# Kernel tuning notes

Hardware: AMD Instinct MI355X
Metric: run time of the kernel (lower is better)

## Reference

```python
import jax, jax.numpy as jnp
import numpy as np

B, S, H = 2, 2048, 4096
NH, NKV, HD = 32, 8, 128
THETA = 1000000.0
NEG = jnp.finfo(jnp.float32).min


def setup_inputs() -> dict:
    key = jax.random.key(0)
    ks = jax.random.split(key, 9)
    s = 0.02
    return {
        "hidden_states": jax.random.normal(ks[0], (B, S, H), jnp.float32),
        "position_ids": jnp.tile(jnp.arange(S, dtype=jnp.int32)[None, :], (B, 1)),
        "Wq": jax.random.normal(ks[1], (NH * HD, H), jnp.float32) * s,
        "bq": jax.random.normal(ks[2], (NH * HD,), jnp.float32) * s,
        "Wk": jax.random.normal(ks[3], (NKV * HD, H), jnp.float32) * s,
        "bk": jax.random.normal(ks[4], (NKV * HD,), jnp.float32) * s,
        "Wv": jax.random.normal(ks[5], (NKV * HD, H), jnp.float32) * s,
        "bv": jax.random.normal(ks[6], (NKV * HD,), jnp.float32) * s,
        "Wo": jax.random.normal(ks[7], (H, H), jnp.float32) * s,
        "bo": jax.random.normal(ks[8], (H,), jnp.float32) * s,
    }


def _rotate_half_interleaved(x):
    # y[..., ::2] = -x[..., 1::2]; y[..., 1::2] = x[..., ::2]
    x2 = x.reshape(*x.shape[:-1], -1, 2)
    y = jnp.stack([-x2[..., 1], x2[..., 0]], axis=-1)
    return y.reshape(x.shape)


def reference(hidden_states, position_ids, Wq, bq, Wk, bk, Wv, bv, Wo, bo):
    bsz, q_len, _ = hidden_states.shape
    q = (hidden_states @ Wq.T + bq).reshape(bsz, q_len, NH, HD).transpose(0, 2, 1, 3)
    k = (hidden_states @ Wk.T + bk).reshape(bsz, q_len, NKV, HD).transpose(0, 2, 1, 3)
    v = (hidden_states @ Wv.T + bv).reshape(bsz, q_len, NKV, HD).transpose(0, 2, 1, 3)

    # rotary embedding (interleaved / repeat_interleave variant)
    inv_freq = 1.0 / (THETA ** (jnp.arange(0, HD, 2, dtype=jnp.float32) / HD))
    freqs = position_ids.astype(jnp.float32)[:, :, None] * inv_freq[None, None, :]  # [B,S,HD/2]
    emb = jnp.repeat(freqs, 2, axis=-1)  # [B,S,HD]
    cos = jnp.cos(emb)[:, None, :, :]  # [B,1,S,HD]
    sin = jnp.sin(emb)[:, None, :, :]
    q = q * cos + _rotate_half_interleaved(q) * sin
    k = k * cos + _rotate_half_interleaved(k) * sin

    # GQA: repeat KV heads (repeat_interleave on head axis)
    n_rep = NH // NKV
    k = jnp.repeat(k, n_rep, axis=1)
    v = jnp.repeat(v, n_rep, axis=1)

    scores = jnp.einsum("bhqd,bhkd->bhqk", q, k) / np.sqrt(HD).astype(np.float32)
    causal = jnp.tril(jnp.ones((q_len, q_len), dtype=bool))
    scores = jnp.where(causal[None, None, :, :], scores, NEG)
    attn = jax.nn.softmax(scores.astype(jnp.float32), axis=-1).astype(q.dtype)
    out = jnp.einsum("bhqk,bhkd->bhqd", attn, v)
    out = out.transpose(0, 2, 1, 3).reshape(bsz, q_len, H)
    return out @ Wo.T + bo
```

## Files before the change

### kernel.cpp

```cpp
#include <hip/hip_runtime.h>
#include <stdint.h>

typedef __bf16 bf16x8 __attribute__((ext_vector_type(8)));
typedef float f32x4 __attribute__((ext_vector_type(4)));
typedef float f32x16 __attribute__((ext_vector_type(16)));

#define S_LEN 2048
#define NKVH 8
#define HDIM 128
#define MROWS 4096
#define LDQKV 6144
#define SCALE 0.08838834764831845f
#define C_LOG2 0.1275405707067851f
#define THR_RAW 62.7f

__device__ __forceinline__ unsigned short f2bf(float f) {
  unsigned u = __float_as_uint(f);
  u += 0x7FFFu + ((u >> 16) & 1u);
  return (unsigned short)(u >> 16);
}
__device__ __forceinline__ float bf2f(unsigned short h) {
  return __uint_as_float(((unsigned)h) << 16);
}

__device__ __forceinline__ void gload16(const unsigned short* g, unsigned short* l) {
  __builtin_amdgcn_global_load_lds(
      (__attribute__((address_space(1))) void*)(g),
      (__attribute__((address_space(3))) void*)(l), 16, 0, 0);
}

__global__ void cast_f32_bf16(const float4* __restrict__ in, ushort4* __restrict__ out, int n4) {
  int i = blockIdx.x * 256 + threadIdx.x;
  const int stride = gridDim.x * 256;
  for (; i < n4; i += stride) {
    float4 v = in[i];
    ushort4 o;
    o.x = f2bf(v.x); o.y = f2bf(v.y); o.z = f2bf(v.z); o.w = f2bf(v.w);
    out[i] = o;
  }
}

template <int OUTF>
__global__ __launch_bounds__(512, 2)
void gemm256(const unsigned short* __restrict__ A,
             const unsigned short* __restrict__ Bw,
             const float* __restrict__ bias,
             void* __restrict__ C,
             int ldc, int K) {
  __shared__ unsigned short lds[2][4][8192];

  const int t = threadIdx.x;
  const int lane = t & 63;
  const int w = t >> 6;
  const int wr = w >> 2, wc = w & 3;
  const int row16 = lane & 15, kgrp = lane >> 4;
  const int m0 = blockIdx.y * 256, n0 = blockIdx.x * 256;

  const int riu = t >> 3;
  const int col = (((t & 7) ^ (riu & 7)) << 3);
  const int rB0 = (riu & 31) + ((riu >> 5) << 6);
  const unsigned short* pA = A + (size_t)(m0 + riu) * K + col;
  const unsigned short* pB = Bw + (size_t)(n0 + rB0) * K + col;

#define STG(nb_, u_, src_)                                                  \
  {                                                                         \
    gload16((src_), &lds[nb_][u_][t * 8]);                                  \
    gload16((src_) + (size_t)128 * K, &lds[nb_][u_][4096 + t * 8]);         \
  }

  const int sw = row16 & 7;
  const int abase = (wr * 64 + row16) * 64;
  const int bbase = (wc * 32 + row16) * 64;

  f32x4 acc[8][4];
#pragma unroll
  for (int i = 0; i < 8; i++)
#pragma unroll
    for (int j = 0; j < 4; j++) acc[i][j] = (f32x4){0.f, 0.f, 0.f, 0.f};

  bf16x8 afr[4][2], bfr[2][2][2];
  const int NT = K >> 6;

  STG(0, 0, pA);
  STG(0, 1, pB);
  STG(0, 2, pB + (size_t)32 * K);
  STG(0, 3, pA + (size_t)64 * K);

  for (int T = 0; T < NT; ++T) {
    const int cb = T & 1, nb = cb ^ 1;
    const unsigned short* Lc = &lds[cb][0][0];
    const size_t kk = (size_t)(T + 1) << 6;
    const bool st = (T + 1 < NT);

    asm volatile("s_waitcnt vmcnt(4)\n\ts_barrier" ::: "memory");
    if (st) STG(nb, 0, pA + kk);
#pragma unroll
    for (int mi = 0; mi < 4; mi++)
#pragma unroll
      for (int ks = 0; ks < 2; ks++)
        afr[mi][ks] = *(const bf16x8*)(Lc + abase + mi * 1024 + ((((ks << 2) + kgrp) ^ sw) << 3));
#pragma unroll
    for (int nj = 0; nj < 2; nj++)
#pragma unroll
      for (int ks = 0; ks < 2; ks++)
        bfr[0][nj][ks] = *(const bf16x8*)(Lc + 8192 + bbase + nj * 1024 + ((((ks << 2) + kgrp) ^ sw) << 3));
    __builtin_amdgcn_s_setprio(1);
#pragma unroll
    for (int mi = 0; mi < 4; mi++)
#pragma unroll
      for (int nj = 0; nj < 2; nj++)
#pragma unroll
        for (int ks = 0; ks < 2; ks++)
          acc[mi][nj] = __builtin_amdgcn_mfma_f32_16x16x32_bf16(afr[mi][ks], bfr[0][nj][ks], acc[mi][nj], 0, 0, 0);
    __builtin_amdgcn_s_setprio(0);

    if (st) {
      asm volatile("s_waitcnt vmcnt(4)\n\ts_barrier" ::: "memory");
      STG(nb, 1, pB + kk);
    } else {
      asm volatile("s_waitcnt vmcnt(2)\n\ts_barrier" ::: "memory");
    }
#pragma unroll
    for (int nj = 0; nj < 2; nj++)
#pragma unroll
      for (int ks = 0; ks < 2; ks++)
        bfr[1][nj][ks] = *(const bf16x8*)(Lc + 16384 + bbase + nj * 1024 + ((((ks << 2) + kgrp) ^ sw) << 3));
    __builtin_amdgcn_s_setprio(1);
#pragma unroll
    for (int mi = 0; mi < 4; mi++)
#pragma unroll
      for (int nj = 0; nj < 2; nj++)
#pragma unroll
        for (int ks = 0; ks < 2; ks++)
          acc[mi][2 + nj] = __builtin_amdgcn_mfma_f32_16x16x32_bf16(afr[mi][ks], bfr[1][nj][ks], acc[mi][2 + nj], 0, 0, 0);
    __builtin_amdgcn_s_setprio(0);

    if (st) {
      asm volatile("s_waitcnt vmcnt(4)\n\ts_barrier" ::: "memory");
      STG(nb, 2, pB + (size_t)32 * K + kk);
    } else {
      asm volatile("s_waitcnt vmcnt(0)\n\ts_barrier" ::: "memory");
    }
#pragma unroll
    for (int mi = 0; mi < 4; mi++)
#pragma unroll
      for (int ks = 0; ks < 2; ks++)
        afr[mi][ks] = *(const bf16x8*)(Lc + 24576 + abase + mi * 1024 + ((((ks << 2) + kgrp) ^ sw) << 3));
    __builtin_amdgcn_s_setprio(1);
#pragma unroll
    for (int mi = 0; mi < 4; mi++)
#pragma unroll
      for (int nj = 0; nj < 2; nj++)
#pragma unroll
        for (int ks = 0; ks < 2; ks++)
          acc[4 + mi][2 + nj] = __builtin_amdgcn_mfma_f32_16x16x32_bf16(afr[mi][ks], bfr[1][nj][ks], acc[4 + mi][2 + nj], 0, 0, 0);
    __builtin_amdgcn_s_setprio(0);

    if (st) {
      asm volatile("s_waitcnt vmcnt(4)\n\ts_barrier" ::: "memory");
      STG(nb, 3, pA + (size_t)64 * K + kk);
    } else {
      asm volatile("s_barrier" ::: "memory");
    }
    __builtin_amdgcn_s_setprio(1);
#pragma unroll
    for (int mi = 0; mi < 4; mi++)
#pragma unroll
      for (int nj = 0; nj < 2; nj++)
#pragma unroll
        for (int ks = 0; ks < 2; ks++)
          acc[4 + mi][nj] = __builtin_amdgcn_mfma_f32_16x16x32_bf16(afr[mi][ks], bfr[0][nj][ks], acc[4 + mi][nj], 0, 0, 0);
    __builtin_amdgcn_s_setprio(0);
  }
#undef STG

#pragma unroll
  for (int MI = 0; MI < 8; MI++) {
#pragma unroll
    for (int NJ = 0; NJ < 4; NJ++) {
      const int gr = m0 + wr * 128 + MI * 16 + kgrp * 4;
      const int gc = n0 + wc * 64 + NJ * 16 + row16;
      const float bv = bias[gc];
#pragma unroll
      for (int jj = 0; jj < 4; jj++) {
        float v = acc[MI][NJ][jj] + bv;
        if (OUTF) ((float*)C)[(size_t)(gr + jj) * ldc + gc] = v;
        else ((unsigned short*)C)[(size_t)(gr + jj) * ldc + gc] = f2bf(v);
      }
    }
  }
}

template <int OUTF>
__global__ __launch_bounds__(512, 2)
void gemm128(const unsigned short* __restrict__ A,
             const unsigned short* __restrict__ Bw,
             const float* __restrict__ bias,
             void* __restrict__ C,
             int ldc, int K) {
  __shared__ unsigned short lds[3 * 24576];

  const int t = threadIdx.x;
  const int lane = t & 63;
  const int w = t >> 6;
  const int wr = w >> 2, wc = w & 3;
  const int row16 = lane & 15, kgrp = lane >> 4;
  const int m0 = blockIdx.y * 128, n0 = blockIdx.x * 256;

  const int riu = t >> 3;
  const int col = (((t & 7) ^ (riu & 7)) << 3);
  const unsigned short* pA = A + (size_t)(m0 + riu) * K + col;
  const unsigned short* pB = Bw + (size_t)(n0 + riu) * K + col;

#define STG6(bo_, kk_)                                                      \
  {                                                                         \
    gload16(pA + (kk_), &lds[(bo_) + t * 8]);                               \
    gload16(pA + (size_t)64 * K + (kk_), &lds[(bo_) + 4096 + t * 8]);       \
    gload16(pB + (kk_), &lds[(bo_) + 8192 + t * 8]);                        \
    gload16(pB + (size_t)64 * K + (kk_), &lds[(bo_) + 12288 + t * 8]);      \
    gload16(pB + (size_t)128 * K + (kk_), &lds[(bo_) + 16384 + t * 8]);     \
    gload16(pB + (size_t)192 * K + (kk_), &lds[(bo_) + 20480 + t * 8]);     \
  }

  const int sw = row16 & 7;
  const int abase = (wr * 64 + row16) * 64;
  const int bbase = 8192 + (wc * 64 + row16) * 64;

  f32x4 acc[4][4];
#pragma unroll
  for (int i = 0; i < 4; i++)
#pragma unroll
    for (int j = 0; j < 4; j++) acc[i][j] = (f32x4){0.f, 0.f, 0.f, 0.f};

  bf16x8 afr[4][2], bfr[4][2];
  const int NT = K >> 6;

  STG6(0, 0);
  STG6(24576, 64);

  int rbc = 0;
  int rbs = 2;
  for (int T = 0; T < NT; ++T) {
    if (T < NT - 1) { asm volatile("s_waitcnt vmcnt(6)\n\ts_barrier" ::: "memory"); }
    else            { asm volatile("s_waitcnt vmcnt(0)\n\ts_barrier" ::: "memory"); }
    if (T + 2 < NT) STG6(rbs * 24576, (size_t)(T + 2) << 6);
    const unsigned short* Lc = &lds[rbc * 24576];

#pragma unroll
    for (int mi = 0; mi < 4; mi++)
#pragma unroll
      for (int ks = 0; ks < 2; ks++)
        afr[mi][ks] = *(const bf16x8*)(Lc + abase + mi * 1024 + ((((ks << 2) + kgrp) ^ sw) << 3));
#pragma unroll
    for (int nj = 0; nj < 4; nj++)
#pragma unroll
      for (int ks = 0; ks < 2; ks++)
        bfr[nj][ks] = *(const bf16x8*)(Lc + bbase + nj * 1024 + ((((ks << 2) + kgrp) ^ sw) << 3));

    __builtin_amdgcn_s_setprio(1);
#pragma unroll
    for (int mi = 0; mi < 4; mi++)
#pragma unroll
      for (int nj = 0; nj < 4; nj++)
#pragma unroll
        for (int ks = 0; ks < 2; ks++)
          acc[mi][nj] = __builtin_amdgcn_mfma_f32_16x16x32_bf16(afr[mi][ks], bfr[nj][ks], acc[mi][nj], 0, 0, 0);
    __builtin_amdgcn_s_setprio(0);

    rbc++; if (rbc == 3) rbc = 0;
    rbs++; if (rbs == 3) rbs = 0;
  }
#undef STG6

#pragma unroll
  for (int MI = 0; MI < 4; MI++) {
#pragma unroll
    for (int NJ = 0; NJ < 4; NJ++) {
      const int gr = m0 + wr * 64 + MI * 16 + kgrp * 4;
      const int gc = n0 + wc * 64 + NJ * 16 + row16;
      const float bv = bias[gc];
#pragma unroll
      for (int jj = 0; jj < 4; jj++) {
        float v = acc[MI][NJ][jj] + bv;
        if (OUTF) ((float*)C)[(size_t)(gr + jj) * ldc + gc] = v;
        else ((unsigned short*)C)[(size_t)(gr + jj) * ldc + gc] = f2bf(v);
      }
    }
  }
}

__global__ void rope_kernel(unsigned short* __restrict__ X,
                            const int* __restrict__ pos_ids,
                            int ncols, int ld) {
  const int perrow = ncols >> 3;
  int idx = blockIdx.x * 256 + threadIdx.x;
  const int row = idx / perrow;
  const int c0 = (idx - row * perrow) << 3;
  const float pos = (float)pos_ids[row];
  unsigned short* p = X + (size_t)row * ld + c0;
  uint4 v = *(uint4*)p;
  unsigned short* e = (unsigned short*)&v;
  const int p0 = (c0 & 127) >> 1;
#pragma unroll
  for (int q = 0; q < 4; ++q) {
    const float inv = exp2f(-(float)(p0 + q) * (19.931568569324174f / 64.f));
    const float fr = pos * inv;
    float sn, cs;
    __sincosf(fr, &sn, &cs);
    const float xe = bf2f(e[2 * q]);
    const float xo = bf2f(e[2 * q + 1]);
    e[2 * q]     = f2bf(xe * cs - xo * sn);
    e[2 * q + 1] = f2bf(xo * cs + xe * sn);
  }
  *(uint4*)p = v;
}

__global__ void transpose_v(const unsigned short* __restrict__ V, int ldv,
                            unsigned short* __restrict__ Vt) {
  __shared__ unsigned short tile[32][40];
  const int t = threadIdx.x;
  const int n0 = blockIdx.x * 32;
  const int m0 = blockIdx.y * 32;
  const int r = t >> 3;
  const int c = (t & 7) << 2;
  const unsigned short* src = V + (size_t)(m0 + r) * ldv + n0 + c;
  ushort4 d = *(const ushort4*)src;
  tile[r][c] = d.x; tile[r][c + 1] = d.y; tile[r][c + 2] = d.z; tile[r][c + 3] = d.w;
  __syncthreads();
  const int b = m0 >> 11;
  unsigned short* dst = Vt + (size_t)(b * 1024 + n0 + r) * 2048 + (m0 & 2047) + c;
  ushort4 o;
  o.x = tile[c][r]; o.y = tile[c + 1][r]; o.z = tile[c + 2][r]; o.w = tile[c + 3][r];
  *(ushort4*)dst = o;
}

__global__ __launch_bounds__(256, 2)
void attn_kernel3(const unsigned short* __restrict__ QKV,
                  const unsigned short* __restrict__ Vt,
                  unsigned short* __restrict__ O) {
  __shared__ unsigned short sK[2 * 64 * 128];
  __shared__ unsigned short sV[2 * 128 * 64];

  const int t = threadIdx.x;
  const int lane = t & 63;
  const int w = t >> 6;
  const int l31 = lane & 31;
  const int hi = lane >> 5;
  const int bid = blockIdx.x;
  const int g = bid >> 6, bh = bid & 63;
  const int qt = (g < 8) ? (15 - g) : (g - 8);
  const int b = bh >> 5, h = bh & 31;
  const int kh = h >> 2;
  const int q0 = qt << 7;
  const int qw = q0 + w * 32;
  const int qg = qw + l31;

  const int ntiles = (q0 + 128) >> 6;
  const int myTiles = (qw + 95) >> 6;

  const int krow0 = t >> 4;
  const int kslot = t & 15;
  const int vrow0 = t >> 3;
  const int vslot = t & 7;
  const unsigned short* Kp = QKV + (size_t)(b * S_LEN) * LDQKV + 4096 + kh * HDIM;
  const unsigned short* Vp = Vt + (size_t)(b * 1024 + kh * HDIM) * 2048;
  const int ksw = (kslot ^ (krow0 & 7)) << 3;
  const int vsw = (vslot ^ (vrow0 & 7)) << 3;
  const unsigned short* KpA = Kp + (size_t)krow0 * LDQKV + ksw;
  const unsigned short* VpA = Vp + (size_t)vrow0 * 2048 + vsw;

#define STAGE(bufi, kv0m)                                                      \
  {                                                                            \
    _Pragma("unroll")                                                          \
    for (int p = 0; p < 4; p++)                                                \
      gload16(KpA + (size_t)((kv0m) + 16 * p) * LDQKV,                         \
              &sK[(bufi) * 8192 + p * 2048 + t * 8]);                          \
    _Pragma("unroll")                                                          \
    for (int p = 0; p < 4; p++)                                                \
      gload16(VpA + (kv0m) + p * 65536, &sV[(bufi) * 8192 + p * 2048 + t * 8]); \
  }

  bf16x8 qf[8];
  {
    const unsigned short* qb = QKV + (size_t)(b * S_LEN + qw + l31) * LDQKV + h * HDIM + hi * 8;
#pragma unroll
    for (int kd = 0; kd < 8; kd++) qf[kd] = *(const bf16x8*)(qb + kd * 16);
  }

  f32x16 o[4];
#pragma unroll
  for (int nt = 0; nt < 4; nt++)
#pragma unroll
    for (int r = 0; r < 16; r++) o[nt][r] = 0.f;
  float m = -1e30f, lsum = 0.f;

  const int rw7 = (l31 & 7) << 4;
  const int kswz = (hi << 4) ^ rw7;
  const int kbase0 = l31 * 128;
  const int vbase = l31 * 64;

  STAGE(0, 0);
  int buf = 0;
  for (int it = 0; it < ntiles; ++it) {
    if (it + 1 < ntiles) {
      STAGE(buf ^ 1, (it + 1) << 6);
      asm volatile("s_waitcnt vmcnt(8)" ::: "memory");
    } else {
      asm volatile("s_waitcnt vmcnt(0)" ::: "memory");
    }
    __builtin_amdgcn_s_barrier();

    if (it < myTiles) {
      const unsigned short* sKc = sK + buf * 8192;
      const unsigned short* sVc = sV + buf * 8192;
      const int kv0 = it << 6;

      f32x16 st[2];
#pragma unroll
      for (int r = 0; r < 16; r++) { st[0][r] = 0.f; st[1][r] = 0.f; }
      __builtin_amdgcn_s_setprio(1);
#pragma unroll
      for (int kd = 0; kd < 8; kd++) {
        bf16x8 k0 = *(const bf16x8*)(sKc + kbase0 + (((kd << 5) ^ kswz) >> 1));
        bf16x8 k1 = *(const bf16x8*)(sKc + 4096 + kbase0 + (((kd << 5) ^ kswz) >> 1));
        st[0] = __builtin_amdgcn_mfma_f32_32x32x16_bf16(k0, qf[kd], st[0], 0, 0, 0);
        st[1] = __builtin_amdgcn_mfma_f32_32x32x16_bf16(k1, qf[kd], st[1], 0, 0, 0);
      }
      __builtin_amdgcn_s_setprio(0);

      if (it == myTiles - 1) {
#pragma unroll
        for (int s2 = 0; s2 < 2; s2++)
#pragma unroll
          for (int r = 0; r < 16; r++) {
            const int kvg = kv0 + s2 * 32 + (r & 3) + 8 * (r >> 2) + 4 * hi;
            if (kvg > qg) st[s2][r] = -1e30f;
          }
      }

      float mx[8];
#pragma unroll
      for (int r = 0; r < 8; r++)
        mx[r] = fmaxf(fmaxf(st[0][r], st[0][r + 8]), fmaxf(st[1][r], st[1][r + 8]));
#pragma unroll
      for (int d = 4; d >= 1; d >>= 1)
#pragma unroll
        for (int r = 0; r < d; r++) mx[r] = fmaxf(mx[r], mx[r + d]);
      float tmax = fmaxf(mx[0], __shfl_xor(mx[0], 32));

      if (!__all(tmax <= m + THR_RAW)) {
        const float mnew = fmaxf(m, tmax);
        const float corr = exp2f((m - mnew) * C_LOG2);
        lsum *= corr;
#pragma unroll
        for (int r = 0; r < 16; r++) {
          const int src = (r & 3) + 8 * (r >> 2) + 4 * hi;
          const float cr = __shfl(corr, src);
#pragma unroll
          for (int nt = 0; nt < 4; nt++) o[nt][r] *= cr;
        }
        m = mnew;
      }
      const float mC = m * C_LOG2;

#pragma unroll
      for (int s2 = 0; s2 < 2; s2++)
#pragma unroll
        for (int r = 0; r < 16; r++) st[s2][r] = exp2f(fmaf(st[s2][r], C_LOG2, -mC));
      float sm[8];
#pragma unroll
      for (int r = 0; r < 8; r++)
        sm[r] = (st[0][r] + st[0][r + 8]) + (st[1][r] + st[1][r + 8]);
#pragma unroll
      for (int d = 4; d >= 1; d >>= 1)
#pragma unroll
        for (int r = 0; r < d; r++) sm[r] += sm[r + d];
      float tsum = sm[0] + __shfl_xor(sm[0], 32);
      lsum += tsum;

      bf16x8 pa[4];
#pragma unroll
      for (int s2 = 0; s2 < 2; s2++) {
        unsigned pw[8];
#pragma unroll
        for (int i = 0; i < 8; i++)
          asm("v_cvt_pk_bf16_f32 %0, %1, %2" : "=v"(pw[i]) : "v"(st[s2][2 * i]), "v"(st[s2][2 * i + 1]));
        const unsigned x0 = (unsigned)__shfl_xor((int)pw[0], 32);
        const unsigned x1 = (unsigned)__shfl_xor((int)pw[1], 32);
        const unsigned x2 = (unsigned)__shfl_xor((int)pw[2], 32);
        const unsigned x3 = (unsigned)__shfl_xor((int)pw[3], 32);
        const unsigned x4 = (unsigned)__shfl_xor((int)pw[4], 32);
        const unsigned x5 = (unsigned)__shfl_xor((int)pw[5], 32);
        const unsigned x6 = (unsigned)__shfl_xor((int)pw[6], 32);
        const unsigned x7 = (unsigned)__shfl_xor((int)pw[7], 32);
        union { unsigned u[4]; bf16x8 v; } u0, u1;
        u0.u[0] = hi ? x2 : pw[0];
        u0.u[1] = hi ? x3 : pw[1];
        u0.u[2] = hi ? pw[2] : x0;
        u0.u[3] = hi ? pw[3] : x1;
        u1.u[0] = hi ? x6 : pw[4];
        u1.u[1] = hi ? x7 : pw[5];
        u1.u[2] = hi ? pw[6] : x4;
        u1.u[3] = hi ? pw[7] : x5;
        pa[2 * s2] = u0.v; pa[2 * s2 + 1] = u1.v;
      }

      __builtin_amdgcn_s_setprio(1);
#pragma unroll
      for (int nt = 0; nt < 4; nt++) {
        const unsigned short* vr = sVc + vbase + nt * 2048;
#pragma unroll
        for (int ks = 0; ks < 4; ks++) {
          bf16x8 vb = *(const bf16x8*)(vr + (((ks << 5) ^ kswz) >> 1));
          o[nt] = __builtin_amdgcn_mfma_f32_32x32x16_bf16(pa[ks], vb, o[nt], 0, 0, 0);
        }
      }
      __builtin_amdgcn_s_setprio(0);
    }

    __builtin_amdgcn_s_barrier();
    buf ^= 1;
  }

  const float linv = 1.0f / lsum;
#pragma unroll
  for (int r = 0; r < 16; r++) {
    const int qr = (r & 3) + 8 * (r >> 2) + 4 * hi;
    const float lr = __shfl(linv, qr);
    unsigned short* orow = O + (size_t)(b * S_LEN + qw + qr) * 4096 + h * HDIM + l31;
#pragma unroll
    for (int nt = 0; nt < 4; nt++) orow[nt * 32] = f2bf(o[nt][r] * lr);
  }
#undef STAGE
}

extern "C" void kernel_launch(void* const* d_in, const int* in_sizes, int n_in,
                              void* d_out, int out_size, void* d_ws, size_t ws_size,
                              hipStream_t stream) {
  const float* hs = (const float*)d_in[0];
  const int*  pos = (const int*)d_in[1];
  const float* Wq = (const float*)d_in[2];
  const float* bq = (const float*)d_in[3];
  const float* Wk = (const float*)d_in[4];
  const float* bk = (const float*)d_in[5];
  const float* Wv = (const float*)d_in[6];
  const float* bv = (const float*)d_in[7];
  const float* Wo = (const float*)d_in[8];
  const float* bo = (const float*)d_in[9];
  float* out = (float*)d_out;

  char* ws = (char*)d_ws;
  unsigned short* hbf  = (unsigned short*)(ws);
  unsigned short* Wbuf = (unsigned short*)(ws + 33554432);
  unsigned short* QKV  = (unsigned short*)(ws + 83886080);
  unsigned short* Vtb  = (unsigned short*)(ws + 134217728);
  float*          biasb= (float*)(ws + 142606336);

  cast_f32_bf16<<<2048, 256, 0, stream>>>((const float4*)hs, (ushort4*)hbf, 4194304);
  cast_f32_bf16<<<2048, 256, 0, stream>>>((const float4*)Wq, (ushort4*)Wbuf, 4194304);
  cast_f32_bf16<<<1024, 256, 0, stream>>>((const float4*)Wk, (ushort4*)(Wbuf + 16777216), 1048576);
  cast_f32_bf16<<<1024, 256, 0, stream>>>((const float4*)Wv, (ushort4*)(Wbuf + 20971520), 1048576);
  hipMemcpyAsync(biasb, bq, 4096 * 4, hipMemcpyDeviceToDevice, stream);
  hipMemcpyAsync(biasb + 4096, bk, 1024 * 4, hipMemcpyDeviceToDevice, stream);
  hipMemcpyAsync(biasb + 5120, bv, 1024 * 4, hipMemcpyDeviceToDevice, stream);

  gemm256<0><<<dim3(16, 16), 512, 0, stream>>>(hbf, Wbuf, biasb, QKV, LDQKV, 4096);
  gemm128<0><<<dim3(8, 32), 512, 0, stream>>>(hbf, Wbuf + 16777216, biasb + 4096, QKV + 4096, LDQKV, 4096);

  cast_f32_bf16<<<2048, 256, 0, stream>>>((const float4*)Wo, (ushort4*)Wbuf, 4194304);

  rope_kernel<<<8192, 256, 0, stream>>>(QKV, pos, 4096, LDQKV);
  rope_kernel<<<2048, 256, 0, stream>>>(QKV + 4096, pos, 1024, LDQKV);

  transpose_v<<<dim3(32, 128), 256, 0, stream>>>(QKV + 5120, LDQKV, Vtb);

  attn_kernel3<<<dim3(1024), 256, 0, stream>>>(QKV, Vtb, hbf);

  gemm256<1><<<dim3(16, 16), 512, 0, stream>>>(hbf, Wbuf, bo, out, 4096, 4096);
}
```

Measured before the change: 520.8 us.

## Restructure GEMM mainloop into 8-slot LDS ring with deeper prefetch

```diff
diff --git a/kernel.cpp b/kernel.cpp
--- a/kernel.cpp
+++ b/kernel.cpp
@@ -47,7 +47,7 @@
              const float* __restrict__ bias,
              void* __restrict__ C,
              int ldc, int K) {
-  __shared__ unsigned short lds[2][4][8192];
+  __shared__ unsigned short lds[8][8192];
 
   const int t = threadIdx.x;
   const int lane = t & 63;
@@ -62,11 +62,30 @@
   const unsigned short* pA = A + (size_t)(m0 + riu) * K + col;
   const unsigned short* pB = Bw + (size_t)(n0 + rB0) * K + col;
 
-#define STG(nb_, u_, src_)                                                  \
+#define STGU(SL, SRC)                                                       \
   {                                                                         \
-    gload16((src_), &lds[nb_][u_][t * 8]);                                  \
-    gload16((src_) + (size_t)128 * K, &lds[nb_][u_][4096 + t * 8]);         \
-  }
+    gload16((SRC), &lds[SL][t * 8]);                                        \
+    gload16((SRC) + (size_t)128 * K, &lds[SL][4096 + t * 8]);               \
+  }
+#define RDA(SL)                                                             \
+  _Pragma("unroll") for (int mi = 0; mi < 4; mi++)                          \
+  _Pragma("unroll") for (int ks = 0; ks < 2; ks++)                          \
+    afr[mi][ks] = *(const bf16x8*)(&lds[SL][0] + abase + mi * 1024 +        \
+                                   ((((ks << 2) + kgrp) ^ sw) << 3));
+#define RDB(SL, W)                                                          \
+  _Pragma("unroll") for (int nj = 0; nj < 2; nj++)                          \
+  _Pragma("unroll") for (int ks = 0; ks < 2; ks++)                          \
+    bfr[W][nj][ks] = *(const bf16x8*)(&lds[SL][0] + bbase + nj * 1024 +     \
+                                      ((((ks << 2) + kgrp) ^ sw) << 3));
+#define MM(MO, NO, W)                                                       \
+  __builtin_amdgcn_s_setprio(1);                                            \
+  _Pragma("unroll") for (int mi = 0; mi < 4; mi++)                          \
+  _Pragma("unroll") for (int nj = 0; nj < 2; nj++)                          \
+  _Pragma("unroll") for (int ks = 0; ks < 2; ks++)                          \
+    acc[(MO) + mi][(NO) + nj] = __builtin_amdgcn_mfma_f32_16x16x32_bf16(    \
+        afr[mi][ks], bfr[W][nj][ks], acc[(MO) + mi][(NO) + nj], 0, 0, 0);   \
+  __builtin_amdgcn_s_setprio(0);
+#define BAR __builtin_amdgcn_s_barrier()
 
   const int sw = row16 & 7;
   const int abase = (wr * 64 + row16) * 64;
@@ -80,99 +99,78 @@
 
   bf16x8 afr[4][2], bfr[2][2][2];
   const int NT = K >> 6;
-
-  STG(0, 0, pA);
-  STG(0, 1, pB);
-  STG(0, 2, pB + (size_t)32 * K);
-  STG(0, 3, pA + (size_t)64 * K);
-
-  for (int T = 0; T < NT; ++T) {
-    const int cb = T & 1, nb = cb ^ 1;
-    const unsigned short* Lc = &lds[cb][0][0];
-    const size_t kk = (size_t)(T + 1) << 6;
-    const bool st = (T + 1 < NT);
-
-    asm volatile("s_waitcnt vmcnt(4)\n\ts_barrier" ::: "memory");
-    if (st) STG(nb, 0, pA + kk);
-#pragma unroll
-    for (int mi = 0; mi < 4; mi++)
-#pragma unroll
-      for (int ks = 0; ks < 2; ks++)
-        afr[mi][ks] = *(const bf16x8*)(Lc + abase + mi * 1024 + ((((ks << 2) + kgrp) ^ sw) << 3));
-#pragma unroll
-    for (int nj = 0; nj < 2; nj++)
-#pragma unroll
-      for (int ks = 0; ks < 2; ks++)
-        bfr[0][nj][ks] = *(const bf16x8*)(Lc + 8192 + bbase + nj * 1024 + ((((ks << 2) + kgrp) ^ sw) << 3));
-    __builtin_amdgcn_s_setprio(1);
-#pragma unroll
-    for (int mi = 0; mi < 4; mi++)
-#pragma unroll
-      for (int nj = 0; nj < 2; nj++)
-#pragma unroll
-        for (int ks = 0; ks < 2; ks++)
-          acc[mi][nj] = __builtin_amdgcn_mfma_f32_16x16x32_bf16(afr[mi][ks], bfr[0][nj][ks], acc[mi][nj], 0, 0, 0);
-    __builtin_amdgcn_s_setprio(0);
-
-    if (st) {
-      asm volatile("s_waitcnt vmcnt(4)\n\ts_barrier" ::: "memory");
-      STG(nb, 1, pB + kk);
+  const int NI = NT >> 1;
+
+  STGU(0, pA);
+  STGU(1, pB);
+  STGU(2, pB + (size_t)32 * K);
+  STGU(3, pA + (size_t)64 * K);
+  STGU(4, pA + 64);
+  STGU(5, pB + 64);
+  STGU(6, pB + (size_t)32 * K + 64);
+  asm volatile("s_waitcnt vmcnt(6)" ::: "memory");
+  BAR;
+
+  for (int I = 0; I < NI; ++I) {
+    const size_t k1 = ((size_t)(2 * I + 1)) << 6;
+    const size_t k2 = ((size_t)(2 * I + 2)) << 6;
+    const size_t k3 = ((size_t)(2 * I + 3)) << 6;
+    const bool s2 = (I + 1 < NI);
+
+    RDA(0); RDB(1, 0);
+    STGU(7, pA + (size_t)64 * K + k1);
+    BAR;
+    MM(0, 0, 0);
+    BAR;
+    RDB(2, 1);
+    if (s2) STGU(0, pA + k2);
+    BAR;
+    MM(0, 2, 1);
+    BAR;
+    RDA(3);
+    if (s2) STGU(1, pB + k2);
+    BAR;
+    MM(4, 2, 1);
+    BAR;
+    if (s2) {
+      STGU(2, pB + (size_t)32 * K + k2);
+      asm volatile("s_waitcnt vmcnt(6)" ::: "memory");
     } else {
-      asm volatile("s_waitcnt vmcnt(2)\n\ts_barrier" ::: "memory");
+      asm volatile("s_waitcnt vmcnt(0)" ::: "memory");
     }
-#pragma unroll
-    for (int nj = 0; nj < 2; nj++)
-#pragma unroll
-      for (int ks = 0; ks < 2; ks++)
-        bfr[1][nj][ks] = *(const bf16x8*)(Lc + 16384 + bbase + nj * 1024 + ((((ks << 2) + kgrp) ^ sw) << 3));
-    __builtin_amdgcn_s_setprio(1);
-#pragma unroll
-    for (int mi = 0; mi < 4; mi++)
-#pragma unroll
-      for (int nj = 0; nj < 2; nj++)
-#pragma unroll
-        for (int ks = 0; ks < 2; ks++)
-          acc[mi][2 + nj] = __builtin_amdgcn_mfma_f32_16x16x32_bf16(afr[mi][ks], bfr[1][nj][ks], acc[mi][2 + nj], 0, 0, 0);
-    __builtin_amdgcn_s_setprio(0);
-
-    if (st) {
-      asm volatile("s_waitcnt vmcnt(4)\n\ts_barrier" ::: "memory");
-      STG(nb, 2, pB + (size_t)32 * K + kk);
+    BAR;
+    MM(4, 0, 0);
+    BAR;
+    RDA(4); RDB(5, 0);
+    if (s2) STGU(3, pA + (size_t)64 * K + k2);
+    BAR;
+    MM(0, 0, 0);
+    BAR;
+    RDB(6, 1);
+    if (s2) STGU(4, pA + k3);
+    BAR;
+    MM(0, 2, 1);
+    BAR;
+    RDA(7);
+    if (s2) STGU(5, pB + k3);
+    BAR;
+    MM(4, 2, 1);
+    BAR;
+    if (s2) {
+      STGU(6, pB + (size_t)32 * K + k3);
+      asm volatile("s_waitcnt vmcnt(6)" ::: "memory");
     } else {
-      asm volatile("s_waitcnt vmcnt(0)\n\ts_barrier" ::: "memory");
+      asm volatile("s_waitcnt vmcnt(0)" ::: "memory");
     }
-#pragma unroll
-    for (int mi = 0; mi < 4; mi++)
-#pragma unroll
-      for (int ks = 0; ks < 2; ks++)
-        afr[mi][ks] = *(const bf16x8*)(Lc + 24576 + abase + mi * 1024 + ((((ks << 2) + kgrp) ^ sw) << 3));
-    __builtin_amdgcn_s_setprio(1);
-#pragma unroll
-    for (int mi = 0; mi < 4; mi++)
-#pragma unroll
-      for (int nj = 0; nj < 2; nj++)
-#pragma unroll
-        for (int ks = 0; ks < 2; ks++)
-          acc[4 + mi][2 + nj] = __builtin_amdgcn_mfma_f32_16x16x32_bf16(afr[mi][ks], bfr[1][nj][ks], acc[4 + mi][2 + nj], 0, 0, 0);
-    __builtin_amdgcn_s_setprio(0);
-
-    if (st) {
-      asm volatile("s_waitcnt vmcnt(4)\n\ts_barrier" ::: "memory");
-      STG(nb, 3, pA + (size_t)64 * K + kk);
-    } else {
-      asm volatile("s_barrier" ::: "memory");
-    }
-    __builtin_amdgcn_s_setprio(1);
-#pragma unroll
-    for (int mi = 0; mi < 4; mi++)
-#pragma unroll
-      for (int nj = 0; nj < 2; nj++)
-#pragma unroll
-        for (int ks = 0; ks < 2; ks++)
-          acc[4 + mi][nj] = __builtin_amdgcn_mfma_f32_16x16x32_bf16(afr[mi][ks], bfr[0][nj][ks], acc[4 + mi][nj], 0, 0, 0);
-    __builtin_amdgcn_s_setprio(0);
-  }
-#undef STG
+    BAR;
+    MM(4, 0, 0);
+    BAR;
+  }
+#undef STGU
+#undef RDA
+#undef RDB
+#undef MM
+#undef BAR
 
 #pragma unroll
   for (int MI = 0; MI < 8; MI++) {
```

Measured after the change: 521.3 us. No clear change (+0.1%).
